# Optimization experiments

Measured on AMD Instinct MI355X. Metric: run time of the kernel, lower is better.

Reference implementation:

```python
import jax, jax.numpy as jnp
import numpy as np

B, K, C, O = 8, 100000, 16, 16
HG, WG = 512, 512
ALPHA_PRIOR = 1.0
KERN = np.array([[0.075, 0.125, 0.075], [0.125, 0.3, 0.125], [0.075, 0.125, 0.075]], dtype=np.float32)


def setup_inputs() -> dict:
    key = jax.random.key(0)
    k1, k2, k3, k4, k5 = jax.random.split(key, 5)
    node_feat = jax.random.normal(k1, (B, K, C), dtype=jnp.float32)
    node_xy = jax.random.uniform(k2, (B, K, 2), dtype=jnp.float32, minval=0.0, maxval=WG - 1.0)
    node_types = jax.random.randint(k3, (B, K), 0, 2)
    # kaiming_normal_ fan_out: std = sqrt(2 / fan_out), fan_out = O*1*1
    std = (2.0 / O) ** 0.5
    w_obj = jax.random.normal(k4, (O, C), dtype=jnp.float32) * std
    w_prior = jax.random.normal(k5, (O, C), dtype=jnp.float32) * std
    hw = np.array([HG, WG], dtype=np.int64)
    return {"node_feat": node_feat, "node_xy": node_xy, "hw": hw,
            "node_types": node_types, "w_obj": w_obj, "w_prior": w_prior}


def rasterize(node_feat, node_xy, weight, H, W):
    # node_feat [B,K,C], node_xy [B,K,2], weight [B,K] 0/1 mask (masked scatter == scatter of zeros)
    xs = jnp.clip(jnp.round(node_xy[..., 0]), 0, W - 1).astype(jnp.int32)
    ys = jnp.clip(jnp.round(node_xy[..., 1]), 0, H - 1).astype(jnp.int32)
    idx = ys * W + xs  # [B,K] flat grid index
    src = node_feat * weight[..., None]  # zero out non-selected nodes

    def scat(idx_b, src_b):
        return jnp.zeros((H * W, src_b.shape[-1]), src_b.dtype).at[idx_b].add(src_b)

    grid = jax.vmap(scat)(idx, src)  # [B,HW,C]
    return grid.reshape(grid.shape[0], H, W, -1).transpose(0, 3, 1, 2)  # [B,C,H,W]


def splat3x3(x, kern):
    # depthwise 3x3 conv, groups = C
    c = x.shape[1]
    w = jnp.broadcast_to(kern[None, None], (c, 1, 3, 3))
    return jax.lax.conv_general_dilated(
        x, w, window_strides=(1, 1), padding='SAME',
        dimension_numbers=('NCHW', 'OIHW', 'NCHW'), feature_group_count=c)


def reference(node_feat, node_xy, hw, node_types, w_obj, w_prior):
    H, W = int(hw[0]), int(hw[1])
    kern = jnp.asarray(KERN)
    mask_obj = (node_types == 0).astype(node_feat.dtype)
    mask_prior = (node_types == 1).astype(node_feat.dtype)
    map_obj = splat3x3(rasterize(node_feat, node_xy, mask_obj, H, W), kern)
    map_prior = splat3x3(rasterize(node_feat, node_xy, mask_prior, H, W), kern)
    # rasterize + splat run under torch.no_grad() in the original
    map_obj = jax.lax.stop_gradient(map_obj)
    map_prior = jax.lax.stop_gradient(map_prior)
    out = jnp.einsum('oc,bchw->bohw', w_obj, map_obj) \
        + ALPHA_PRIOR * jnp.einsum('oc,bchw->bohw', w_prior, map_prior)
    return out
```

## Files before the change

### kernel.cpp

```cpp
#include <hip/hip_runtime.h>

#define B_ 8
#define K_ 100000
#define NODES (B_ * K_)
#define C_ 16
#define O_ 16
#define H_ 512
#define W_ 512
#define TSX 32
#define TSY 16
#define NTX (W_ / TSX)
#define NTY (H_ / TSY)
#define NBKT (B_ * NTX * NTY)
#define CAP 512
#define EX (TSX + 2)
#define EY (TSY + 2)
#define PLANE (EX * EY)
#define FILL_BLOCKS 64
#define CHUNK (NODES / FILL_BLOCKS)
#define CUR_OFF 256
#define IDS_OFF 32768

__device__ __forceinline__ float bf_lo(unsigned int u) {
    union { unsigned int i; float f; } v; v.i = u << 16; return v.f;
}
__device__ __forceinline__ float bf_hi(unsigned int u) {
    union { unsigned int i; float f; } v; v.i = u & 0xffff0000u; return v.f;
}
__device__ __forceinline__ unsigned short f2bf(float f) {
    union { float f; unsigned int u; } v; v.f = f;
    unsigned int u = v.u;
    u += 0x7fffu + ((u >> 16) & 1u);
    return (unsigned short)(u >> 16);
}

__global__ void detect_fp32(const unsigned int* __restrict__ xy, int* __restrict__ flag)
{
    __shared__ int bad;
    if (threadIdx.x == 0) bad = 0;
    __syncthreads();
    unsigned int u = xy[threadIdx.x];
    float lo = bf_lo(u);
    if (!(lo >= 0.0f && lo <= 512.0f)) bad = 1;
    __syncthreads();
    if (threadIdx.x == 0) *flag = bad;
}

__device__ __forceinline__ void decode_xy(const void* xy, int fp32, int n,
                                          int& xs, int& ys)
{
    float x, y;
    if (fp32) { float2 p = ((const float2*)xy)[n]; x = p.x; y = p.y; }
    else { unsigned int u = ((const unsigned int*)xy)[n]; x = bf_lo(u); y = bf_hi(u); }
    xs = min(max((int)rintf(x), 0), W_ - 1);
    ys = min(max((int)rintf(y), 0), H_ - 1);
}

__global__ __launch_bounds__(256) void fill_bins(
    const void* __restrict__ xy, const int* __restrict__ flag,
    int* __restrict__ cursor, int* __restrict__ ids)
{
    __shared__ int hist[NBKT];
    const int fp32 = *flag;
    for (int j = threadIdx.x; j < NBKT; j += 256) hist[j] = 0;
    __syncthreads();

    const int s = blockIdx.x * CHUNK, e = s + CHUNK;

    for (int i = s + threadIdx.x; i < e; i += 256) {
        int xs, ys; decode_xy(xy, fp32, i, xs, ys);
        int bb = i / K_;
        int xlo = max((xs - 1) >> 5, 0), xhi = min((xs + 1) >> 5, NTX - 1);
        int ylo = max((ys - 1) >> 4, 0), yhi = min((ys + 1) >> 4, NTY - 1);
        for (int tyy = ylo; tyy <= yhi; ++tyy)
            for (int txx = xlo; txx <= xhi; ++txx)
                atomicAdd(&hist[(bb * NTY + tyy) * NTX + txx], 1);
    }
    __syncthreads();

    for (int j = threadIdx.x; j < NBKT; j += 256) {
        int c = hist[j];
        hist[j] = c ? atomicAdd(&cursor[j], c) : 0;
    }
    __syncthreads();

    for (int i = s + threadIdx.x; i < e; i += 256) {
        int xs, ys; decode_xy(xy, fp32, i, xs, ys);
        int bb = i / K_;
        int xlo = max((xs - 1) >> 5, 0), xhi = min((xs + 1) >> 5, NTX - 1);
        int ylo = max((ys - 1) >> 4, 0), yhi = min((ys + 1) >> 4, NTY - 1);
        for (int tyy = ylo; tyy <= yhi; ++tyy)
            for (int txx = xlo; txx <= xhi; ++txx) {
                int bk = (bb * NTY + tyy) * NTX + txx;
                int slot = atomicAdd(&hist[bk], 1);
                if (slot < CAP) ids[bk * CAP + slot] = i;
            }
    }
}

__global__ __launch_bounds__(512) void tile_fused(
    const void* __restrict__ feat, const void* __restrict__ xy,
    const int* __restrict__ types,
    const void* __restrict__ w_obj, const void* __restrict__ w_prior,
    const int* __restrict__ flag,
    const int* __restrict__ cursor, const int* __restrict__ ids,
    void* __restrict__ out)
{
    __shared__ float accs[O_ * PLANE];
    __shared__ float wl[2 * O_ * C_];
    const int fp32 = *flag;

    const int tx = blockIdx.x, ty = blockIdx.y, b = blockIdx.z;
    const int x0 = tx * TSX, y0 = ty * TSY;
    const int bucket = (b * NTY + ty) * NTX + tx;

    for (int i = threadIdx.x; i < O_ * PLANE; i += 512) accs[i] = 0.f;
    if (fp32) {
        for (int i = threadIdx.x; i < 2 * O_ * C_; i += 512)
            wl[i] = (i < O_ * C_) ? ((const float*)w_obj)[i]
                                  : ((const float*)w_prior)[i - O_ * C_];
    } else {
        for (int i = threadIdx.x; i < 2 * O_ * C_; i += 512) {
            unsigned short raw = (i < O_ * C_)
                ? ((const unsigned short*)w_obj)[i]
                : ((const unsigned short*)w_prior)[i - O_ * C_];
            union { unsigned int u; float f; } v; v.u = ((unsigned int)raw) << 16;
            wl[i] = v.f;
        }
    }
    __syncthreads();

    int cnt = cursor[bucket];
    if (cnt > CAP) cnt = CAP;

    for (int i = threadIdx.x; i < cnt; i += 512) {
        int n = ids[bucket * CAP + i];
        int xs, ys; decode_xy(xy, fp32, n, xs, ys);
        int lx = xs - x0 + 1, ly = ys - y0 + 1;

        float f[16];
        if (fp32) {
            const float4* ff = (const float4*)feat + (size_t)n * 4;
            float4 a = ff[0], bb = ff[1], c = ff[2], d = ff[3];
            f[0]=a.x; f[1]=a.y; f[2]=a.z; f[3]=a.w;
            f[4]=bb.x; f[5]=bb.y; f[6]=bb.z; f[7]=bb.w;
            f[8]=c.x; f[9]=c.y; f[10]=c.z; f[11]=c.w;
            f[12]=d.x; f[13]=d.y; f[14]=d.z; f[15]=d.w;
        } else {
            const uint4* ff = (const uint4*)feat + (size_t)n * 2;
            uint4 A = ff[0], Bv = ff[1];
            f[0]=bf_lo(A.x);  f[1]=bf_hi(A.x);  f[2]=bf_lo(A.y);  f[3]=bf_hi(A.y);
            f[4]=bf_lo(A.z);  f[5]=bf_hi(A.z);  f[6]=bf_lo(A.w);  f[7]=bf_hi(A.w);
            f[8]=bf_lo(Bv.x); f[9]=bf_hi(Bv.x); f[10]=bf_lo(Bv.y); f[11]=bf_hi(Bv.y);
            f[12]=bf_lo(Bv.z); f[13]=bf_hi(Bv.z); f[14]=bf_lo(Bv.w); f[15]=bf_hi(Bv.w);
        }

        const float* wrow = &wl[(types[n] != 0) ? O_ * C_ : 0];
        float* cell = &accs[ly * EX + lx];
        #pragma unroll
        for (int o = 0; o < O_; ++o) {
            float acc = 0.f;
            #pragma unroll
            for (int c = 0; c < C_; ++c) acc = fmaf(wrow[o * C_ + c], f[c], acc);
            atomicAdd(cell + o * PLANE, acc);
        }
    }
    __syncthreads();

    const int x = threadIdx.x & 31;
    const int o = threadIdx.x >> 5;
    const float* pl = &accs[o * PLANE + x];
    float hA2 = 0.f, hA1 = 0.f, hB1 = 0.f;
    const size_t obase = (((size_t)(b * O_ + o)) * H_) * W_;

    #pragma unroll
    for (int iy = 0; iy < EY; ++iy) {
        float l = pl[iy * EX], c = pl[iy * EX + 1], r = pl[iy * EX + 2];
        float sfx = l + r;
        float hA = fmaf(0.075f, sfx, 0.125f * c);
        float hB = fmaf(0.125f, sfx, 0.3f * c);
        if (iy >= 2) {
            float v = hA2 + hB1 + hA;
            size_t oi = obase + (size_t)(y0 + iy - 2) * W_ + (x0 + x);
            if (fp32) ((float*)out)[oi] = v;
            else      ((unsigned short*)out)[oi] = f2bf(v);
        }
        hA2 = hA1; hA1 = hA; hB1 = hB;
    }
}

extern "C" void kernel_launch(void* const* d_in, const int* in_sizes, int n_in,
                              void* d_out, int out_size, void* d_ws, size_t ws_size,
                              hipStream_t stream)
{
    const void* feat = d_in[0];
    const void* xy = d_in[1];
    const int* types = (const int*)d_in[3];
    const void* w_obj = d_in[4];
    const void* w_prior = d_in[5];

    int* flag = (int*)d_ws;
    int* cursor = (int*)((char*)d_ws + CUR_OFF);
    int* ids = (int*)((char*)d_ws + IDS_OFF);

    detect_fp32<<<1, 256, 0, stream>>>((const unsigned int*)xy, flag);
    hipMemsetAsync(cursor, 0, NBKT * sizeof(int), stream);
    fill_bins<<<FILL_BLOCKS, 256, 0, stream>>>(xy, flag, cursor, ids);
    tile_fused<<<dim3(NTX, NTY, B_), 512, 0, stream>>>(
        feat, xy, types, w_obj, w_prior, flag, cursor, ids, d_out);
}
```

Measured before the change: 342.1 us.

## Pack local coords and type into bin ids, inline dtype probe, widen fill grid

Each bin entry now packs the node's local index, type bit and tile-local lx/ly, so the tile kernel no longer gathers xy and types per node. The separate fp32-detect kernel is removed and every block reruns the probe itself. fill_bins now uses 256 per-batch blocks with a small per-block histogram and caches decoded coordinates in shared memory between its two passes. Output stores become nontemporal. This removes one launch and the random gathers, at the cost of redundant probe work in every block and tighter bit-packing limits on the id fields.

```diff
diff --git a/kernel.cpp b/kernel.cpp
--- a/kernel.cpp
+++ b/kernel.cpp
@@ -16,10 +16,9 @@
 #define EX (TSX + 2)
 #define EY (TSY + 2)
 #define PLANE (EX * EY)
-#define FILL_BLOCKS 64
-#define CHUNK (NODES / FILL_BLOCKS)
-#define CUR_OFF 256
-#define IDS_OFF 32768
+#define FB 256
+#define FCHUNK (K_ / (FB / B_))
+#define IDS_OFF 16384
 
 __device__ __forceinline__ float bf_lo(unsigned int u) {
     union { unsigned int i; float f; } v; v.i = u << 16; return v.f;
@@ -34,16 +33,14 @@
     return (unsigned short)(u >> 16);
 }
 
-__global__ void detect_fp32(const unsigned int* __restrict__ xy, int* __restrict__ flag)
-{
-    __shared__ int bad;
-    if (threadIdx.x == 0) bad = 0;
-    __syncthreads();
-    unsigned int u = xy[threadIdx.x];
-    float lo = bf_lo(u);
-    if (!(lo >= 0.0f && lo <= 512.0f)) bad = 1;
-    __syncthreads();
-    if (threadIdx.x == 0) *flag = bad;
+__device__ __forceinline__ void probe_fp32(const unsigned int* xy, int tid,
+                                           int* bad )
+{
+    if (tid == 0) *bad = 0;
+    if (tid < 256) {
+        float lo = bf_lo(xy[tid]);
+        if (!(lo >= 0.0f && lo <= 512.0f)) *bad = 1;
+    }
 }
 
 __device__ __forceinline__ void decode_xy(const void* xy, int fp32, int n,
@@ -57,70 +54,89 @@
 }
 
 __global__ __launch_bounds__(256) void fill_bins(
-    const void* __restrict__ xy, const int* __restrict__ flag,
+    const void* __restrict__ xy, const int* __restrict__ types,
     int* __restrict__ cursor, int* __restrict__ ids)
 {
-    __shared__ int hist[NBKT];
-    const int fp32 = *flag;
-    for (int j = threadIdx.x; j < NBKT; j += 256) hist[j] = 0;
-    __syncthreads();
-
-    const int s = blockIdx.x * CHUNK, e = s + CHUNK;
-
-    for (int i = s + threadIdx.x; i < e; i += 256) {
-        int xs, ys; decode_xy(xy, fp32, i, xs, ys);
-        int bb = i / K_;
+    __shared__ int hist[NTX * NTY];
+    __shared__ unsigned int rec[FCHUNK];
+    __shared__ int bad;
+
+    const int tid = threadIdx.x;
+    probe_fp32((const unsigned int*)xy, tid, &bad);
+    for (int j = tid; j < NTX * NTY; j += 256) hist[j] = 0;
+    __syncthreads();
+    const int fp32 = bad;
+
+    const int bb = blockIdx.x >> 5;
+    const int local0 = (blockIdx.x & 31) * FCHUNK;
+    const int s = bb * K_ + local0;
+
+    for (int ii = tid; ii < FCHUNK; ii += 256) {
+        int n = s + ii;
+        int xs, ys; decode_xy(xy, fp32, n, xs, ys);
+        int t = (types[n] != 0);
+        rec[ii] = (unsigned)(xs | (ys << 9) | (t << 18));
         int xlo = max((xs - 1) >> 5, 0), xhi = min((xs + 1) >> 5, NTX - 1);
         int ylo = max((ys - 1) >> 4, 0), yhi = min((ys + 1) >> 4, NTY - 1);
         for (int tyy = ylo; tyy <= yhi; ++tyy)
             for (int txx = xlo; txx <= xhi; ++txx)
-                atomicAdd(&hist[(bb * NTY + tyy) * NTX + txx], 1);
-    }
-    __syncthreads();
-
-    for (int j = threadIdx.x; j < NBKT; j += 256) {
+                atomicAdd(&hist[tyy * NTX + txx], 1);
+    }
+    __syncthreads();
+
+    for (int j = tid; j < NTX * NTY; j += 256) {
         int c = hist[j];
-        hist[j] = c ? atomicAdd(&cursor[j], c) : 0;
-    }
-    __syncthreads();
-
-    for (int i = s + threadIdx.x; i < e; i += 256) {
-        int xs, ys; decode_xy(xy, fp32, i, xs, ys);
-        int bb = i / K_;
+        hist[j] = c ? atomicAdd(&cursor[bb * NTX * NTY + j], c) : 0;
+    }
+    __syncthreads();
+
+    for (int ii = tid; ii < FCHUNK; ii += 256) {
+        unsigned r = rec[ii];
+        int xs = r & 511, ys = (r >> 9) & 511, t = (r >> 18) & 1;
+        int local = local0 + ii;
         int xlo = max((xs - 1) >> 5, 0), xhi = min((xs + 1) >> 5, NTX - 1);
         int ylo = max((ys - 1) >> 4, 0), yhi = min((ys + 1) >> 4, NTY - 1);
         for (int tyy = ylo; tyy <= yhi; ++tyy)
             for (int txx = xlo; txx <= xhi; ++txx) {
-                int bk = (bb * NTY + tyy) * NTX + txx;
+                int bk = tyy * NTX + txx;
                 int slot = atomicAdd(&hist[bk], 1);
-                if (slot < CAP) ids[bk * CAP + slot] = i;
+                if (slot < CAP) {
+                    int lx = xs - (txx << 5) + 1;
+                    int ly = ys - (tyy << 4) + 1;
+                    ids[(bb * NTX * NTY + bk) * CAP + slot] =
+                        local | (t << 17) | (lx << 18) | (ly << 24);
+                }
             }
     }
 }
 
 __global__ __launch_bounds__(512) void tile_fused(
     const void* __restrict__ feat, const void* __restrict__ xy,
-    const int* __restrict__ types,
     const void* __restrict__ w_obj, const void* __restrict__ w_prior,
-    const int* __restrict__ flag,
     const int* __restrict__ cursor, const int* __restrict__ ids,
     void* __restrict__ out)
 {
     __shared__ float accs[O_ * PLANE];
     __shared__ float wl[2 * O_ * C_];
-    const int fp32 = *flag;
-
+    __shared__ int bad;
+
+    const int tid = threadIdx.x;
     const int tx = blockIdx.x, ty = blockIdx.y, b = blockIdx.z;
-    const int x0 = tx * TSX, y0 = ty * TSY;
     const int bucket = (b * NTY + ty) * NTX + tx;
-
-    for (int i = threadIdx.x; i < O_ * PLANE; i += 512) accs[i] = 0.f;
+    int cnt = cursor[bucket];
+    if (cnt > CAP) cnt = CAP;
+
+    probe_fp32((const unsigned int*)xy, tid, &bad);
+    for (int i = tid; i < O_ * PLANE; i += 512) accs[i] = 0.f;
+    __syncthreads();
+    const int fp32 = bad;
+
     if (fp32) {
-        for (int i = threadIdx.x; i < 2 * O_ * C_; i += 512)
+        for (int i = tid; i < 2 * O_ * C_; i += 512)
             wl[i] = (i < O_ * C_) ? ((const float*)w_obj)[i]
                                   : ((const float*)w_prior)[i - O_ * C_];
     } else {
-        for (int i = threadIdx.x; i < 2 * O_ * C_; i += 512) {
+        for (int i = tid; i < 2 * O_ * C_; i += 512) {
             unsigned short raw = (i < O_ * C_)
                 ? ((const unsigned short*)w_obj)[i]
                 : ((const unsigned short*)w_prior)[i - O_ * C_];
@@ -130,24 +146,24 @@
     }
     __syncthreads();
 
-    int cnt = cursor[bucket];
-    if (cnt > CAP) cnt = CAP;
-
-    for (int i = threadIdx.x; i < cnt; i += 512) {
-        int n = ids[bucket * CAP + i];
-        int xs, ys; decode_xy(xy, fp32, n, xs, ys);
-        int lx = xs - x0 + 1, ly = ys - y0 + 1;
+    for (int i = tid; i < cnt; i += 512) {
+        unsigned p = (unsigned)ids[bucket * CAP + i];
+        int local = p & 0x1FFFF;
+        int t  = (p >> 17) & 1;
+        int lx = (p >> 18) & 63;
+        int ly = (p >> 24) & 31;
+        size_t n = (size_t)b * K_ + local;
 
         float f[16];
         if (fp32) {
-            const float4* ff = (const float4*)feat + (size_t)n * 4;
-            float4 a = ff[0], bb = ff[1], c = ff[2], d = ff[3];
+            const float4* ff = (const float4*)feat + n * 4;
+            float4 a = ff[0], bb2 = ff[1], c = ff[2], d = ff[3];
             f[0]=a.x; f[1]=a.y; f[2]=a.z; f[3]=a.w;
-            f[4]=bb.x; f[5]=bb.y; f[6]=bb.z; f[7]=bb.w;
+            f[4]=bb2.x; f[5]=bb2.y; f[6]=bb2.z; f[7]=bb2.w;
             f[8]=c.x; f[9]=c.y; f[10]=c.z; f[11]=c.w;
             f[12]=d.x; f[13]=d.y; f[14]=d.z; f[15]=d.w;
         } else {
-            const uint4* ff = (const uint4*)feat + (size_t)n * 2;
+            const uint4* ff = (const uint4*)feat + n * 2;
             uint4 A = ff[0], Bv = ff[1];
             f[0]=bf_lo(A.x);  f[1]=bf_hi(A.x);  f[2]=bf_lo(A.y);  f[3]=bf_hi(A.y);
             f[4]=bf_lo(A.z);  f[5]=bf_hi(A.z);  f[6]=bf_lo(A.w);  f[7]=bf_hi(A.w);
@@ -155,7 +171,7 @@
             f[12]=bf_lo(Bv.z); f[13]=bf_hi(Bv.z); f[14]=bf_lo(Bv.w); f[15]=bf_hi(Bv.w);
         }
 
-        const float* wrow = &wl[(types[n] != 0) ? O_ * C_ : 0];
+        const float* wrow = &wl[t * O_ * C_];
         float* cell = &accs[ly * EX + lx];
         #pragma unroll
         for (int o = 0; o < O_; ++o) {
@@ -167,10 +183,11 @@
     }
     __syncthreads();
 
-    const int x = threadIdx.x & 31;
-    const int o = threadIdx.x >> 5;
+    const int x = tid & 31;
+    const int o = tid >> 5;
     const float* pl = &accs[o * PLANE + x];
     float hA2 = 0.f, hA1 = 0.f, hB1 = 0.f;
+    const int x0 = tx * TSX, y0 = ty * TSY;
     const size_t obase = (((size_t)(b * O_ + o)) * H_) * W_;
 
     #pragma unroll
@@ -182,8 +199,8 @@
         if (iy >= 2) {
             float v = hA2 + hB1 + hA;
             size_t oi = obase + (size_t)(y0 + iy - 2) * W_ + (x0 + x);
-            if (fp32) ((float*)out)[oi] = v;
-            else      ((unsigned short*)out)[oi] = f2bf(v);
+            if (fp32) __builtin_nontemporal_store(v, (float*)out + oi);
+            else      __builtin_nontemporal_store(f2bf(v), (unsigned short*)out + oi);
         }
         hA2 = hA1; hA1 = hA; hB1 = hB;
     }
@@ -199,13 +216,11 @@
     const void* w_obj = d_in[4];
     const void* w_prior = d_in[5];
 
-    int* flag = (int*)d_ws;
-    int* cursor = (int*)((char*)d_ws + CUR_OFF);
+    int* cursor = (int*)d_ws;
     int* ids = (int*)((char*)d_ws + IDS_OFF);
 
-    detect_fp32<<<1, 256, 0, stream>>>((const unsigned int*)xy, flag);
     hipMemsetAsync(cursor, 0, NBKT * sizeof(int), stream);
-    fill_bins<<<FILL_BLOCKS, 256, 0, stream>>>(xy, flag, cursor, ids);
+    fill_bins<<<FB, 256, 0, stream>>>(xy, types, cursor, ids);
     tile_fused<<<dim3(NTX, NTY, B_), 512, 0, stream>>>(
-        feat, xy, types, w_obj, w_prior, flag, cursor, ids, d_out);
-}
+        feat, xy, w_obj, w_prior, cursor, ids, d_out);
+}
```

After: 287.1 us. 16.1% less time.
